# Performance work log

Measured on AMD Instinct MI355X. Metric: run time of the kernel, lower is better.

Reference implementation:

```python
import jax, jax.numpy as jnp
import numpy as np

DIM = 64  # head dim, init arg
SCALE = DIM ** -0.5

def setup_inputs() -> dict:
    key = jax.random.key(0)
    kq, kk, kv = jax.random.split(key, 3)
    shape = (4, 2048, 8, 64)  # (b, n, h, d)
    q = jax.random.normal(kq, shape, dtype=jnp.float32)
    k = jax.random.normal(kk, shape, dtype=jnp.float32)
    v = jax.random.normal(kv, shape, dtype=jnp.float32)
    return {"q": q, "k": k, "v": v}

def reference(q, k, v):
    # score: [b, h, n_q, n_k] -- matches torch bmm over (b*h) batched [n, d] x [d, n]
    score = jnp.einsum('bqhd,bkhd->bhqk', q, k) * SCALE
    attn = jax.nn.softmax(score, axis=-1)
    # context back to [b, n, h, d] (torch permutes h,b,n,d -> b,n,h,d)
    context = jnp.einsum('bhqk,bkhd->bqhd', attn, v)
    return context
```

## Files before the change

kernel.cpp:

```cpp
#include <hip/hip_runtime.h>

#define B 4
#define N 2048
#define H 8
#define D 64
#define HD 512
#define QT 128
#define KT 64
#define NT2 16
#define PLS 72

typedef _Float16 half8 __attribute__((ext_vector_type(8)));
typedef float float4_ __attribute__((ext_vector_type(4)));
typedef float float16_ __attribute__((ext_vector_type(16)));

#define MFMA32(a, b, c) __builtin_amdgcn_mfma_f32_32x32x16_f16((a), (b), (c), 0, 0, 0)

__global__ void prep_kernel(const float* __restrict__ K, const float* __restrict__ V,
                            _Float16* __restrict__ Kf, _Float16* __restrict__ Vtr) {
    __shared__ _Float16 tile[64][PLS];
    const int t = threadIdx.x;
    if (blockIdx.x < 2048) {
        const size_t i = (size_t)blockIdx.x * 256 + t;
        const float4_* p = (const float4_*)(K + i * 8);
        float4_ a = p[0], b = p[1];
        half8 hh;
        #pragma unroll
        for (int j = 0; j < 4; ++j) { hh[j] = (_Float16)a[j]; hh[4 + j] = (_Float16)b[j]; }
        *(half8*)(Kf + i * 8) = hh;
    } else {
        const int bid = blockIdx.x - 2048;
        const int nt = bid & 31, h = (bid >> 5) & 7, b = bid >> 8;
        {
            const int i = t >> 2, c0 = (t & 3) * 16;
            const float* vp = V + (size_t)b * N * HD + (size_t)(nt * 64 + i) * HD + h * D + c0;
            #pragma unroll
            for (int j = 0; j < 4; ++j) {
                float4_ a = *(const float4_*)(vp + j * 4);
                #pragma unroll
                for (int c = 0; c < 4; ++c) tile[i][c0 + j * 4 + c] = (_Float16)a[c];
            }
        }
        __syncthreads();
        {
            const int d = t >> 2, n0 = (t & 3) * 16;
            half8 w0, w1;
            #pragma unroll
            for (int j = 0; j < 4; ++j) {
                w0[j]     = tile[n0 + j][d];
                w0[4 + j] = tile[n0 + 8 + j][d];
                w1[j]     = tile[n0 + 4 + j][d];
                w1[4 + j] = tile[n0 + 12 + j][d];
            }
            _Float16* op = Vtr + ((size_t)(b * H + h) * D + d) * N + nt * 64 + n0;
            *(half8*)op = w0;
            *(half8*)(op + 8) = w1;
        }
    }
}

__device__ __forceinline__ void stage_k(const _Float16* __restrict__ Kbh, int keybase,
                                        _Float16* kb, int wg, int lane) {
    const int rsub = lane >> 3, slot = lane & 7;
    #pragma unroll
    for (int i = 0; i < 2; ++i) {
        const int row = wg * 16 + i * 8 + rsub;
        const int c = slot ^ (row & 7);
        __builtin_amdgcn_global_load_lds(
            (const __attribute__((address_space(1))) void*)(Kbh + (size_t)(keybase + row) * HD + c * 8),
            (__attribute__((address_space(3))) void*)(kb + (wg * 16 + i * 8) * 64), 16, 0, 0);
    }
}
__device__ __forceinline__ void stage_v(const _Float16* __restrict__ Vbh, int keybase,
                                        _Float16* vb, int wg, int lane) {
    const int rsub = lane >> 3, slot = lane & 7;
    #pragma unroll
    for (int i = 0; i < 2; ++i) {
        const int row = wg * 16 + i * 8 + rsub;
        const int c = slot ^ (row & 7);
        __builtin_amdgcn_global_load_lds(
            (const __attribute__((address_space(1))) void*)(Vbh + (size_t)row * N + keybase + c * 8),
            (__attribute__((address_space(3))) void*)(vb + (wg * 16 + i * 8) * 64), 16, 0, 0);
    }
}

#define DO_S_HALF(KC, KB, PA, PB)                                              \
    {                                                                          \
        float16_ s = {};                                                       \
        __builtin_amdgcn_s_setprio(1);                                         \
        _Pragma("unroll")                                                      \
        for (int ks = 0; ks < 4; ++ks) {                                       \
            const int csw = ((2 * ks + hi) ^ (ln & 7)) * 8;                    \
            half8 a = *(const half8*)((KC) + ((KB) * 32 + ln) * 64 + csw);     \
            s = MFMA32(a, qf[ks], s);                                          \
        }                                                                      \
        __builtin_amdgcn_s_setprio(0);                                         \
        half8 f0, f1;                                                          \
        _Pragma("unroll")                                                      \
        for (int j = 0; j < 8; ++j) {                                          \
            float pa_ = __builtin_amdgcn_exp2f(s[j]);                          \
            float pb_ = __builtin_amdgcn_exp2f(s[8 + j]);                      \
            ls0 += pa_; ls1 += pb_;                                            \
            f0[j] = (_Float16)pa_;                                             \
            f1[j] = (_Float16)pb_;                                             \
        }                                                                      \
        PA = f0; PB = f1;                                                      \
    }

#define PV_STEP(VC, KS, P)                                                     \
    {                                                                          \
        const int csw = ((2 * (KS) + hi) ^ (ln & 7)) * 8;                      \
        half8 b0 = *(const half8*)((VC) + ln * 64 + csw);                      \
        half8 b1 = *(const half8*)((VC) + (32 + ln) * 64 + csw);               \
        o0 = MFMA32(P, b0, o0);                                                \
        o1 = MFMA32(P, b1, o1);                                                \
    }

#define DO_PV(VC, P0, P1, P2, P3)                                              \
    __builtin_amdgcn_s_setprio(1);                                             \
    PV_STEP(VC, 0, P0) PV_STEP(VC, 1, P1)                                      \
    PV_STEP(VC, 2, P2) PV_STEP(VC, 3, P3)                                      \
    __builtin_amdgcn_s_setprio(0);

#define PHASE(T, C0, C1, C2, C3, Pp0, Pp1, Pp2, Pp3, WITHPV)                   \
    {                                                                          \
        if ((T) < NT2 - 1) asm volatile("s_waitcnt vmcnt(4)" ::: "memory");    \
        else               asm volatile("s_waitcnt vmcnt(0)" ::: "memory");    \
        __builtin_amdgcn_s_barrier();                                          \
        __builtin_amdgcn_sched_barrier(0);                                     \
        const _Float16* kc_ = Kb + ((T) & 1) * 4096;                           \
        DO_S_HALF(kc_, 0, C0, C1)                                              \
        DO_S_HALF(kc_, 1, C2, C3)                                              \
        if (WITHPV) {                                                          \
            const _Float16* vp_ = Vb + (((T) + 2) % 3) * 4096;                 \
            DO_PV(vp_, Pp0, Pp1, Pp2, Pp3)                                     \
        }                                                                      \
        if ((T) + 2 < NT2) {                                                   \
            __builtin_amdgcn_s_barrier();                                      \
            __builtin_amdgcn_sched_barrier(0);                                 \
            stage_k(Kbh, tbase + ((T) + 2) * KT, Kb + ((T) & 1) * 4096, qg, lane); \
            stage_v(Vbh, tbase + ((T) + 2) * KT, Vb + (((T) + 2) % 3) * 4096, qg, lane); \
        }                                                                      \
    }

__global__ __launch_bounds__(512, 2)
void fattn13_kernel(const float* __restrict__ Q, const _Float16* __restrict__ Kf,
                    const _Float16* __restrict__ Vt, float* __restrict__ Out)
{
    static __shared__ __align__(16) _Float16 smem[40960];

    const int tid  = threadIdx.x;
    const int wave = tid >> 6;
    const int lane = tid & 63;
    const int ln   = lane & 31;
    const int hi   = lane >> 5;
    const int qg   = wave & 3;
    const int kh   = wave >> 2;

    const int h = blockIdx.y;
    const int b = blockIdx.z;
    const int q_base = blockIdx.x * QT + qg * 32;

    const size_t bh_q = (size_t)b * N * HD + (size_t)h * D;
    const _Float16* Kbh = Kf + bh_q;
    const _Float16* Vbh = Vt + (size_t)(b * H + h) * D * N;

    _Float16* Kb = smem + kh * 8192;
    _Float16* Vb = smem + 16384 + kh * 12288;

    const float SC = 0.125f * 1.4426950408889634f;
    half8 qf[4];
    {
        const float* qp = Q + bh_q + (size_t)(q_base + ln) * HD + hi * 8;
        #pragma unroll
        for (int ks = 0; ks < 4; ++ks) {
            float4_ a0 = *(const float4_*)(qp + ks * 16);
            float4_ a1 = *(const float4_*)(qp + ks * 16 + 4);
            half8 f;
            #pragma unroll
            for (int j = 0; j < 4; ++j) { f[j] = (_Float16)(a0[j] * SC); f[4 + j] = (_Float16)(a1[j] * SC); }
            qf[ks] = f;
        }
    }

    float16_ o0 = {}, o1 = {};
    float ls0 = 0.f, ls1 = 0.f;
    half8 pa0, pa1, pa2, pa3;
    half8 pb0, pb1, pb2, pb3;

    const int tbase = kh * NT2 * KT;

    stage_k(Kbh, tbase, Kb, qg, lane);              stage_v(Vbh, tbase, Vb, qg, lane);
    stage_k(Kbh, tbase + KT, Kb + 4096, qg, lane);  stage_v(Vbh, tbase + KT, Vb + 4096, qg, lane);

    PHASE(0, pa0, pa1, pa2, pa3, pb0, pb1, pb2, pb3, false)
    for (int t = 1; t < NT2 - 1; t += 2) {
        PHASE(t,     pb0, pb1, pb2, pb3, pa0, pa1, pa2, pa3, true)
        PHASE(t + 1, pa0, pa1, pa2, pa3, pb0, pb1, pb2, pb3, true)
    }
    PHASE(NT2 - 1, pb0, pb1, pb2, pb3, pa0, pa1, pa2, pa3, true)
    {
        const _Float16* vp_ = Vb + ((NT2 - 1) % 3) * 4096;
        DO_PV(vp_, pb0, pb1, pb2, pb3)
    }
    float lsum = ls0 + ls1;

    __syncthreads();
    float* cb = (float*)smem;
    float* ls = cb + 4 * 2 * 16 * 64;
    if (kh == 1) {
        #pragma unroll
        for (int r = 0; r < 16; ++r) {
            cb[((qg * 2 + 0) * 16 + r) * 64 + lane] = o0[r];
            cb[((qg * 2 + 1) * 16 + r) * 64 + lane] = o1[r];
        }
        ls[qg * 64 + lane] = lsum;
    }
    __syncthreads();
    if (kh == 0) {
        #pragma unroll
        for (int r = 0; r < 16; ++r) {
            o0[r] += cb[((qg * 2 + 0) * 16 + r) * 64 + lane];
            o1[r] += cb[((qg * 2 + 1) * 16 + r) * 64 + lane];
        }
        lsum += ls[qg * 64 + lane];
        float v = lsum;
        v += __shfl_xor(v, 32, 64);
        const float inv = 1.0f / v;
        #pragma unroll
        for (int r = 0; r < 16; ++r) {
            const int rl = (r & 3) + 8 * (r >> 2) + 4 * hi;
            const float linv = __shfl(inv, rl, 64);
            const size_t ro = bh_q + (size_t)(q_base + rl) * HD;
            Out[ro + ln]      = o0[r] * linv;
            Out[ro + 32 + ln] = o1[r] * linv;
        }
    }
}

__global__ __launch_bounds__(256, 2)
void fattn_fb_kernel(const float* __restrict__ Q, const float* __restrict__ K,
                     const float* __restrict__ V, float* __restrict__ Out)
{
    __shared__ __align__(16) _Float16 Ks[KT][PLS];
    __shared__ __align__(16) _Float16 Vts[D][PLS];
    __shared__ __align__(16) _Float16 Pwf[4][16][PLS];
    const int tid = threadIdx.x, wave = tid >> 6, lane = tid & 63;
    const int m = lane & 15, quad = lane >> 4;
    const int q_base = blockIdx.x * 64;
    const size_t bh_off = ((size_t)blockIdx.z * N * H + (size_t)blockIdx.y) * D;
    const float SCALE = 0.125f;
    const int qrow = q_base + wave * 16 + m;
    const float* qp = Q + bh_off + (size_t)qrow * HD + quad * 8;
    half8 qf0, qf1;
    #pragma unroll
    for (int j = 0; j < 8; ++j) qf0[j] = (_Float16)(qp[j] * SCALE);
    #pragma unroll
    for (int j = 0; j < 8; ++j) qf1[j] = (_Float16)(qp[32 + j] * SCALE);
    float4_ o[4] = {};
    float mi[4], li[4];
    #pragma unroll
    for (int r = 0; r < 4; ++r) { mi[r] = -1e30f; li[r] = 0.0f; }
    for (int kt = 0; kt < N; kt += KT) {
        __syncthreads();
        {
            const int key = tid >> 2, c0 = (tid & 3) * 16;
            const float* kp = K + bh_off + (size_t)(kt + key) * HD + c0;
            half8 lo, hi;
            #pragma unroll
            for (int j = 0; j < 8; ++j) lo[j] = (_Float16)kp[j];
            #pragma unroll
            for (int j = 0; j < 8; ++j) hi[j] = (_Float16)kp[8 + j];
            *(half8*)&Ks[key][c0] = lo;
            *(half8*)&Ks[key][c0 + 8] = hi;
        }
        {
            const int c0 = (tid & 15) * 4, k0 = (tid >> 4) * 4;
            const float* vp = V + bh_off + (size_t)(kt + k0) * HD + c0;
            #pragma unroll
            for (int c = 0; c < 4; ++c)
                #pragma unroll
                for (int i = 0; i < 4; ++i)
                    Vts[c0 + c][k0 + i] = (_Float16)vp[i * HD + c];
        }
        __syncthreads();
        float4_ s[4];
        #pragma unroll
        for (int blk = 0; blk < 4; ++blk) {
            const int key = blk * 16 + m;
            half8 kf0 = *(const half8*)&Ks[key][quad * 8];
            half8 kf1 = *(const half8*)&Ks[key][32 + quad * 8];
            float4_ acc = {};
            acc = __builtin_amdgcn_mfma_f32_16x16x32_f16(qf0, kf0, acc, 0, 0, 0);
            acc = __builtin_amdgcn_mfma_f32_16x16x32_f16(qf1, kf1, acc, 0, 0, 0);
            s[blk] = acc;
        }
        float alpha[4];
        #pragma unroll
        for (int r = 0; r < 4; ++r) {
            float v0 = fmaxf(fmaxf(s[0][r], s[1][r]), fmaxf(s[2][r], s[3][r]));
            #pragma unroll
            for (int mask = 1; mask < 16; mask <<= 1) v0 = fmaxf(v0, __shfl_xor(v0, mask, 64));
            float mn = fmaxf(mi[r], v0);
            alpha[r] = __expf(mi[r] - mn);
            mi[r] = mn;
        }
        #pragma unroll
        for (int blk = 0; blk < 4; ++blk)
            #pragma unroll
            for (int r = 0; r < 4; ++r) s[blk][r] = __expf(s[blk][r] - mi[r]);
        #pragma unroll
        for (int r = 0; r < 4; ++r) {
            float tt = s[0][r] + s[1][r] + s[2][r] + s[3][r];
            #pragma unroll
            for (int mask = 1; mask < 16; mask <<= 1) tt += __shfl_xor(tt, mask, 64);
            li[r] = li[r] * alpha[r] + tt;
        }
        #pragma unroll
        for (int d = 0; d < 4; ++d)
            #pragma unroll
            for (int r = 0; r < 4; ++r) o[d][r] *= alpha[r];
        #pragma unroll
        for (int blk = 0; blk < 4; ++blk)
            #pragma unroll
            for (int r = 0; r < 4; ++r)
                Pwf[wave][quad * 4 + r][blk * 16 + m] = (_Float16)s[blk][r];
        #pragma unroll
        for (int ks = 0; ks < 2; ++ks) {
            half8 af = *(const half8*)&Pwf[wave][m][ks * 32 + quad * 8];
            #pragma unroll
            for (int d = 0; d < 4; ++d) {
                half8 bf = *(const half8*)&Vts[d * 16 + m][ks * 32 + quad * 8];
                o[d] = __builtin_amdgcn_mfma_f32_16x16x32_f16(af, bf, o[d], 0, 0, 0);
            }
        }
    }
    #pragma unroll
    for (int d = 0; d < 4; ++d)
        #pragma unroll
        for (int r = 0; r < 4; ++r) {
            const int row = q_base + wave * 16 + quad * 4 + r;
            Out[bh_off + (size_t)row * HD + d * 16 + m] = o[d][r] / li[r];
        }
}

extern "C" void kernel_launch(void* const* d_in, const int* in_sizes, int n_in,
                              void* d_out, int out_size, void* d_ws, size_t ws_size,
                              hipStream_t stream) {
    const float* q = (const float*)d_in[0];
    const float* k = (const float*)d_in[1];
    const float* v = (const float*)d_in[2];
    float* out = (float*)d_out;

    const size_t nelem = (size_t)B * N * H * D;
    const size_t need = 2 * nelem * sizeof(_Float16);

    if (ws_size >= need) {
        _Float16* Kf = (_Float16*)d_ws;
        _Float16* Vtr = Kf + nelem;
        prep_kernel<<<dim3(2048 + 1024), 256, 0, stream>>>(k, v, Kf, Vtr);
        fattn13_kernel<<<dim3(N / QT, H, B), 512, 0, stream>>>(q, Kf, Vtr, out);
    } else {
        fattn_fb_kernel<<<dim3(N / 64, H, B), 256, 0, stream>>>(q, k, v, out);
    }
}
```

Baseline: 140.6 us.

## Pre-pack K/V into MFMA fragment order and load fragments directly from global

```diff
diff --git a/kernel.cpp b/kernel.cpp
--- a/kernel.cpp
+++ b/kernel.cpp
@@ -9,6 +9,7 @@
 #define KT 64
 #define NT2 16
 #define PLS 72
+#define HEADE 131072
 
 typedef _Float16 half8 __attribute__((ext_vector_type(8)));
 typedef float float4_ __attribute__((ext_vector_type(4)));
@@ -16,20 +17,30 @@
 
 #define MFMA32(a, b, c) __builtin_amdgcn_mfma_f32_32x32x16_f16((a), (b), (c), 0, 0, 0)
 
-__global__ void prep_kernel(const float* __restrict__ K, const float* __restrict__ V,
-                            _Float16* __restrict__ Kf, _Float16* __restrict__ Vtr) {
+__global__ void prep2_kernel(const float* __restrict__ K, const float* __restrict__ V,
+                             _Float16* __restrict__ Kt2, _Float16* __restrict__ Vt2) {
     __shared__ _Float16 tile[64][PLS];
     const int t = threadIdx.x;
-    if (blockIdx.x < 2048) {
-        const size_t i = (size_t)blockIdx.x * 256 + t;
-        const float4_* p = (const float4_*)(K + i * 8);
-        float4_ a = p[0], b = p[1];
-        half8 hh;
-        #pragma unroll
-        for (int j = 0; j < 4; ++j) { hh[j] = (_Float16)a[j]; hh[4 + j] = (_Float16)b[j]; }
-        *(half8*)(Kf + i * 8) = hh;
+    if (blockIdx.x < 1024) {
+        const int bid = blockIdx.x;
+        const int tt = bid & 31, h = (bid >> 5) & 7, b = bid >> 8;
+        const size_t src = (size_t)b * N * HD + (size_t)h * D;
+        const size_t dst = (size_t)(b * H + h) * HEADE;
+        const int c  = t >> 4;
+        const int lp = (t & 15) * 2;
+        #pragma unroll
+        for (int i = 0; i < 2; ++i) {
+            const int l = lp + i;
+            const int row = tt * 64 + (c >> 3) * 32 + l;
+            const float* sp = K + src + (size_t)row * HD + (c & 7) * 8;
+            float4_ a0 = *(const float4_*)sp, a1 = *(const float4_*)(sp + 4);
+            half8 f;
+            #pragma unroll
+            for (int j = 0; j < 4; ++j) { f[j] = (_Float16)a0[j]; f[4 + j] = (_Float16)a1[j]; }
+            *(half8*)(Kt2 + dst + ((size_t)(tt * 16 + c) * 32 + l) * 8) = f;
+        }
     } else {
-        const int bid = blockIdx.x - 2048;
+        const int bid = blockIdx.x - 1024;
         const int nt = bid & 31, h = (bid >> 5) & 7, b = bid >> 8;
         {
             const int i = t >> 2, c0 = (t & 3) * 16;
@@ -38,7 +49,7 @@
             for (int j = 0; j < 4; ++j) {
                 float4_ a = *(const float4_*)(vp + j * 4);
                 #pragma unroll
-                for (int c = 0; c < 4; ++c) tile[i][c0 + j * 4 + c] = (_Float16)a[c];
+                for (int cc = 0; cc < 4; ++cc) tile[i][c0 + j * 4 + cc] = (_Float16)a[cc];
             }
         }
         __syncthreads();
@@ -52,102 +63,83 @@
                 w1[j]     = tile[n0 + 4 + j][d];
                 w1[4 + j] = tile[n0 + 12 + j][d];
             }
-            _Float16* op = Vtr + ((size_t)(b * H + h) * D + d) * N + nt * 64 + n0;
+            const int c0 = (t & 3) * 2;
+            _Float16* op = Vt2 + (size_t)(b * H + h) * HEADE
+                               + (size_t)(nt * 8 + c0) * 512 + d * 8;
             *(half8*)op = w0;
-            *(half8*)(op + 8) = w1;
+            *(half8*)(op + 512) = w1;
         }
     }
 }
 
-__device__ __forceinline__ void stage_k(const _Float16* __restrict__ Kbh, int keybase,
-                                        _Float16* kb, int wg, int lane) {
-    const int rsub = lane >> 3, slot = lane & 7;
-    #pragma unroll
-    for (int i = 0; i < 2; ++i) {
-        const int row = wg * 16 + i * 8 + rsub;
-        const int c = slot ^ (row & 7);
-        __builtin_amdgcn_global_load_lds(
-            (const __attribute__((address_space(1))) void*)(Kbh + (size_t)(keybase + row) * HD + c * 8),
-            (__attribute__((address_space(3))) void*)(kb + (wg * 16 + i * 8) * 64), 16, 0, 0);
-    }
-}
-__device__ __forceinline__ void stage_v(const _Float16* __restrict__ Vbh, int keybase,
-                                        _Float16* vb, int wg, int lane) {
-    const int rsub = lane >> 3, slot = lane & 7;
-    #pragma unroll
-    for (int i = 0; i < 2; ++i) {
-        const int row = wg * 16 + i * 8 + rsub;
-        const int c = slot ^ (row & 7);
-        __builtin_amdgcn_global_load_lds(
-            (const __attribute__((address_space(1))) void*)(Vbh + (size_t)row * N + keybase + c * 8),
-            (__attribute__((address_space(3))) void*)(vb + (wg * 16 + i * 8) * 64), 16, 0, 0);
-    }
-}
-
-#define DO_S_HALF(KC, KB, PA, PB)                                              \
+#define DO_S_HALF(TT, KB, PA, PB)                                              \
     {                                                                          \
-        float16_ s = {};                                                       \
+        const _Float16* kp_ = Kb2 + ((size_t)((TT) * 16 + (KB) * 8 + hi) * 32 + ln) * 8; \
+        half8 a0_ = *(const half8*)(kp_);                                      \
+        half8 a1_ = *(const half8*)(kp_ + 512);                                \
+        half8 a2_ = *(const half8*)(kp_ + 1024);                               \
+        half8 a3_ = *(const half8*)(kp_ + 1536);                               \
+        float16_ s_ = {};                                                      \
         __builtin_amdgcn_s_setprio(1);                                         \
-        _Pragma("unroll")                                                      \
-        for (int ks = 0; ks < 4; ++ks) {                                       \
-            const int csw = ((2 * ks + hi) ^ (ln & 7)) * 8;                    \
-            half8 a = *(const half8*)((KC) + ((KB) * 32 + ln) * 64 + csw);     \
-            s = MFMA32(a, qf[ks], s);                                          \
-        }                                                                      \
+        s_ = MFMA32(a0_, qf[0], s_);                                           \
+        s_ = MFMA32(a1_, qf[1], s_);                                           \
+        s_ = MFMA32(a2_, qf[2], s_);                                           \
+        s_ = MFMA32(a3_, qf[3], s_);                                           \
         __builtin_amdgcn_s_setprio(0);                                         \
-        half8 f0, f1;                                                          \
+        half8 f0_, f1_;                                                        \
         _Pragma("unroll")                                                      \
         for (int j = 0; j < 8; ++j) {                                          \
-            float pa_ = __builtin_amdgcn_exp2f(s[j]);                          \
-            float pb_ = __builtin_amdgcn_exp2f(s[8 + j]);                      \
+            float pa_ = __builtin_amdgcn_exp2f(s_[j]);                         \
+            float pb_ = __builtin_amdgcn_exp2f(s_[8 + j]);                     \
             ls0 += pa_; ls1 += pb_;                                            \
-            f0[j] = (_Float16)pa_;                                             \
-            f1[j] = (_Float16)pb_;                                             \
+            f0_[j] = (_Float16)pa_;                                            \
+            f1_[j] = (_Float16)pb_;                                            \
         }                                                                      \
-        PA = f0; PB = f1;                                                      \
-    }
-
-#define PV_STEP(VC, KS, P)                                                     \
+        PA = f0_; PB = f1_;                                                    \
+    }
+
+#define LOAD_V01(TT)                                                           \
     {                                                                          \
-        const int csw = ((2 * (KS) + hi) ^ (ln & 7)) * 8;                      \
-        half8 b0 = *(const half8*)((VC) + ln * 64 + csw);                      \
-        half8 b1 = *(const half8*)((VC) + (32 + ln) * 64 + csw);               \
-        o0 = MFMA32(P, b0, o0);                                                \
-        o1 = MFMA32(P, b1, o1);                                                \
-    }
-
-#define DO_PV(VC, P0, P1, P2, P3)                                              \
+        const _Float16* vp_ = Vb2 + (size_t)((TT) * 8 + hi) * 512 + ln * 8;    \
+        v00 = *(const half8*)(vp_);                                            \
+        v01 = *(const half8*)(vp_ + 256);                                      \
+        v10 = *(const half8*)(vp_ + 1024);                                     \
+        v11 = *(const half8*)(vp_ + 1280);                                     \
+    }
+#define LOAD_V23(TT)                                                           \
+    {                                                                          \
+        const _Float16* vp_ = Vb2 + (size_t)((TT) * 8 + hi) * 512 + ln * 8;    \
+        v20 = *(const half8*)(vp_ + 2048);                                     \
+        v21 = *(const half8*)(vp_ + 2304);                                     \
+        v30 = *(const half8*)(vp_ + 3072);                                     \
+        v31 = *(const half8*)(vp_ + 3328);                                     \
+    }
+#define PV01(P0, P1)                                                           \
     __builtin_amdgcn_s_setprio(1);                                             \
-    PV_STEP(VC, 0, P0) PV_STEP(VC, 1, P1)                                      \
-    PV_STEP(VC, 2, P2) PV_STEP(VC, 3, P3)                                      \
+    o0 = MFMA32(P0, v00, o0); o1 = MFMA32(P0, v01, o1);                        \
+    o0 = MFMA32(P1, v10, o0); o1 = MFMA32(P1, v11, o1);                        \
     __builtin_amdgcn_s_setprio(0);
-
-#define PHASE(T, C0, C1, C2, C3, Pp0, Pp1, Pp2, Pp3, WITHPV)                   \
+#define PV23(P2, P3)                                                           \
+    __builtin_amdgcn_s_setprio(1);                                             \
+    o0 = MFMA32(P2, v20, o0); o1 = MFMA32(P2, v21, o1);                        \
+    o0 = MFMA32(P3, v30, o0); o1 = MFMA32(P3, v31, o1);                        \
+    __builtin_amdgcn_s_setprio(0);
+
+#define PHASE_PV(T, C0, C1, C2, C3, Pp0, Pp1, Pp2, Pp3)                        \
     {                                                                          \
-        if ((T) < NT2 - 1) asm volatile("s_waitcnt vmcnt(4)" ::: "memory");    \
-        else               asm volatile("s_waitcnt vmcnt(0)" ::: "memory");    \
-        __builtin_amdgcn_s_barrier();                                          \
-        __builtin_amdgcn_sched_barrier(0);                                     \
-        const _Float16* kc_ = Kb + ((T) & 1) * 4096;                           \
-        DO_S_HALF(kc_, 0, C0, C1)                                              \
-        DO_S_HALF(kc_, 1, C2, C3)                                              \
-        if (WITHPV) {                                                          \
-            const _Float16* vp_ = Vb + (((T) + 2) % 3) * 4096;                 \
-            DO_PV(vp_, Pp0, Pp1, Pp2, Pp3)                                     \
-        }                                                                      \
-        if ((T) + 2 < NT2) {                                                   \
-            __builtin_amdgcn_s_barrier();                                      \
-            __builtin_amdgcn_sched_barrier(0);                                 \
-            stage_k(Kbh, tbase + ((T) + 2) * KT, Kb + ((T) & 1) * 4096, qg, lane); \
-            stage_v(Vbh, tbase + ((T) + 2) * KT, Vb + (((T) + 2) % 3) * 4096, qg, lane); \
-        }                                                                      \
+        LOAD_V01(kh16 + (T) - 1)                                               \
+        DO_S_HALF(kh16 + (T), 0, C0, C1)                                       \
+        PV01(Pp0, Pp1)                                                         \
+        LOAD_V23(kh16 + (T) - 1)                                               \
+        DO_S_HALF(kh16 + (T), 1, C2, C3)                                       \
+        PV23(Pp2, Pp3)                                                         \
     }
 
 __global__ __launch_bounds__(512, 2)
-void fattn13_kernel(const float* __restrict__ Q, const _Float16* __restrict__ Kf,
-                    const _Float16* __restrict__ Vt, float* __restrict__ Out)
+void fattn15_kernel(const float* __restrict__ Q, const _Float16* __restrict__ Kt2,
+                    const _Float16* __restrict__ Vt2, float* __restrict__ Out)
 {
-    static __shared__ __align__(16) _Float16 smem[40960];
+    __shared__ float cbuf[8448];
 
     const int tid  = threadIdx.x;
     const int wave = tid >> 6;
@@ -156,17 +148,16 @@
     const int hi   = lane >> 5;
     const int qg   = wave & 3;
     const int kh   = wave >> 2;
+    const int kh16 = kh * 16;
 
     const int h = blockIdx.y;
     const int b = blockIdx.z;
     const int q_base = blockIdx.x * QT + qg * 32;
 
     const size_t bh_q = (size_t)b * N * HD + (size_t)h * D;
-    const _Float16* Kbh = Kf + bh_q;
-    const _Float16* Vbh = Vt + (size_t)(b * H + h) * D * N;
-
-    _Float16* Kb = smem + kh * 8192;
-    _Float16* Vb = smem + 16384 + kh * 12288;
+    const size_t headb = (size_t)(b * H + h) * HEADE;
+    const _Float16* Kb2 = Kt2 + headb;
+    const _Float16* Vb2 = Vt2 + headb;
 
     const float SC = 0.125f * 1.4426950408889634f;
     half8 qf[4];
@@ -187,27 +178,24 @@
     float ls0 = 0.f, ls1 = 0.f;
     half8 pa0, pa1, pa2, pa3;
     half8 pb0, pb1, pb2, pb3;
-
-    const int tbase = kh * NT2 * KT;
-
-    stage_k(Kbh, tbase, Kb, qg, lane);              stage_v(Vbh, tbase, Vb, qg, lane);
-    stage_k(Kbh, tbase + KT, Kb + 4096, qg, lane);  stage_v(Vbh, tbase + KT, Vb + 4096, qg, lane);
-
-    PHASE(0, pa0, pa1, pa2, pa3, pb0, pb1, pb2, pb3, false)
+    half8 v00, v01, v10, v11, v20, v21, v30, v31;
+
+    DO_S_HALF(kh16, 0, pa0, pa1)
+    DO_S_HALF(kh16, 1, pa2, pa3)
     for (int t = 1; t < NT2 - 1; t += 2) {
-        PHASE(t,     pb0, pb1, pb2, pb3, pa0, pa1, pa2, pa3, true)
-        PHASE(t + 1, pa0, pa1, pa2, pa3, pb0, pb1, pb2, pb3, true)
-    }
-    PHASE(NT2 - 1, pb0, pb1, pb2, pb3, pa0, pa1, pa2, pa3, true)
-    {
-        const _Float16* vp_ = Vb + ((NT2 - 1) % 3) * 4096;
-        DO_PV(vp_, pb0, pb1, pb2, pb3)
-    }
+        PHASE_PV(t,     pb0, pb1, pb2, pb3, pa0, pa1, pa2, pa3)
+        PHASE_PV(t + 1, pa0, pa1, pa2, pa3, pb0, pb1, pb2, pb3)
+    }
+    PHASE_PV(NT2 - 1, pb0, pb1, pb2, pb3, pa0, pa1, pa2, pa3)
+    LOAD_V01(kh16 + NT2 - 1)
+    PV01(pb0, pb1)
+    LOAD_V23(kh16 + NT2 - 1)
+    PV23(pb2, pb3)
     float lsum = ls0 + ls1;
 
     __syncthreads();
-    float* cb = (float*)smem;
-    float* ls = cb + 4 * 2 * 16 * 64;
+    float* cb = cbuf;
+    float* ls = cbuf + 8192;
     if (kh == 1) {
         #pragma unroll
         for (int r = 0; r < 16; ++r) {
@@ -356,10 +344,10 @@
     const size_t need = 2 * nelem * sizeof(_Float16);
 
     if (ws_size >= need) {
-        _Float16* Kf = (_Float16*)d_ws;
-        _Float16* Vtr = Kf + nelem;
-        prep_kernel<<<dim3(2048 + 1024), 256, 0, stream>>>(k, v, Kf, Vtr);
-        fattn13_kernel<<<dim3(N / QT, H, B), 512, 0, stream>>>(q, Kf, Vtr, out);
+        _Float16* Kt2 = (_Float16*)d_ws;
+        _Float16* Vt2 = Kt2 + nelem;
+        prep2_kernel<<<dim3(2048), 256, 0, stream>>>(k, v, Kt2, Vt2);
+        fattn15_kernel<<<dim3(N / QT, H, B), 512, 0, stream>>>(q, Kt2, Vt2, out);
     } else {
         fattn_fb_kernel<<<dim3(N / 64, H, B), 256, 0, stream>>>(q, k, v, out);
     }
```

Result: no change. 140.7 us (+0.0%).
